# Kernel optimization log

Hardware: AMD Instinct MI355X
Metric: run time of the kernel (lower is better)

The kernel has to match this reference:

```python
import jax, jax.numpy as jnp
import numpy as np
import math

# hyperparams matching init_kwargs
GAMMA_S = 0.8
GAMMA_U = 0.8
RHO_I = 0.1
RHO_T = 0.1
EPS = 1e-10
TAU_MIN = 0.005
TAU_MAX = 1.0
TAU_INIT = 0.07
GRAD_CLIP = 5.0
ETA_INIT = 0.01
ETA_MIN = 0.0001
N_STATE = 2900000
BSZ = 4096
DIM = 1024


def setup_inputs() -> dict:
    key = jax.random.key(0)
    k1, k2 = jax.random.split(key)
    imf = jax.random.normal(k1, (BSZ, DIM), jnp.float32)
    imf = imf / jnp.linalg.norm(imf, axis=1, keepdims=True)
    txf = jax.random.normal(k2, (BSZ, DIM), jnp.float32)
    txf = txf / jnp.linalg.norm(txf, axis=1, keepdims=True)
    return {
        "image_features": imf,
        "text_features": txf,
        "s_I": jnp.zeros((N_STATE,), jnp.float32),
        "s_T": jnp.zeros((N_STATE,), jnp.float32),
        "tau_I": jnp.full((N_STATE,), TAU_INIT, jnp.float32),
        "tau_T": jnp.full((N_STATE,), TAU_INIT, jnp.float32),
        "u_I": jnp.zeros((N_STATE,), jnp.float32),
        "u_T": jnp.zeros((N_STATE,), jnp.float32),
        "b_I": jnp.zeros((N_STATE,), jnp.float32),
        "b_T": jnp.zeros((N_STATE,), jnp.float32),
        "image_ids": jnp.arange(BSZ, dtype=jnp.int32),
        "text_ids": jnp.arange(BSZ, dtype=jnp.int32),
        "epoch": 5,
        "max_epoch": 30,
    }


def reference(image_features, text_features, s_I, s_T, tau_I, tau_T,
              u_I, u_T, b_I, b_T, image_ids, text_ids, epoch, max_epoch):
    B = image_features.shape[0]
    sim = jnp.einsum('id,jd->ij', image_features, text_features)  # [B,B]
    diag_sim = jnp.diagonal(sim)                                  # [B]

    tau_image = tau_I[image_ids]  # [B]
    tau_text = tau_T[text_ids]    # [B]

    image_diffs = sim - diag_sim[:, None]
    text_diffs = sim - diag_sim[None, :]
    # .detach() in torch -> stop_gradient
    idt = jax.lax.stop_gradient(image_diffs / tau_image[:, None])
    tdt = jax.lax.stop_gradient(text_diffs / tau_text[None, :])

    # max-trick state b_I / b_T: running row/col max per sample id
    old_b_I = b_I[image_ids]
    new_b_I = jnp.maximum(jnp.max(idt, axis=1), old_b_I)  # [B]
    old_b_T = b_T[text_ids]
    new_b_T = jnp.maximum(jnp.max(tdt, axis=0), old_b_T)  # [B]

    exp_image_diffs = jnp.exp(idt - new_b_I[:, None])
    exp_text_diffs = jnp.exp(tdt - new_b_T[None, :])
    g_I = jnp.sum(exp_image_diffs, axis=1, keepdims=True) / (B - 1)  # [B,1]
    g_T = jnp.sum(exp_text_diffs, axis=0, keepdims=True) / (B - 1)   # [1,B]

    # moving-average s state (compute_last=False, last_g_* = None path)
    s_I_new = (1.0 - GAMMA_S) * s_I[image_ids] * jnp.exp(old_b_I - new_b_I) + GAMMA_S * g_I[:, 0]
    s_T_new = (1.0 - GAMMA_S) * s_T[text_ids] * jnp.exp(old_b_T - new_b_T) + GAMMA_S * g_T[0, :]
    s_I_b = s_I_new[:, None]  # same shape as g_I
    s_T_b = s_T_new[None, :]  # same shape as g_T

    weights_image = exp_image_diffs / (s_I_b + EPS)
    weights_text = exp_text_diffs / (s_T_b + EPS)

    image_loss = jnp.sum(weights_image * image_diffs, axis=1, keepdims=True) / (B - 1)
    text_loss = jnp.sum(weights_text * text_diffs, axis=0, keepdims=True) / (B - 1)
    total_loss = image_loss.mean() + text_loss.mean()

    grad_tau_image = (jnp.log(s_I_b) + new_b_I[:, None] + RHO_I
                      - jnp.sum(weights_image * idt, axis=1, keepdims=True) / (B - 1))
    grad_tau_text = (jnp.log(s_T_b) + new_b_T[None, :] + RHO_T
                     - jnp.sum(weights_text * tdt, axis=0, keepdims=True) / (B - 1))

    u_I_new = (1.0 - GAMMA_U) * u_I[image_ids] + GAMMA_U * jnp.clip(grad_tau_image[:, 0], -GRAD_CLIP, GRAD_CLIP)
    u_T_new = (1.0 - GAMMA_U) * u_T[text_ids] + GAMMA_U * jnp.clip(grad_tau_text[0, :], -GRAD_CLIP, GRAD_CLIP)

    eta_cur = ETA_MIN + (ETA_INIT - ETA_MIN) * math.cos(math.pi * (epoch / max_epoch) / 2)
    tau_I_new = jnp.clip(tau_image - eta_cur * u_I_new, TAU_MIN, TAU_MAX)
    tau_T_new = jnp.clip(tau_text - eta_cur * u_T_new, TAU_MIN, TAU_MAX)

    # scattered state writes (the module's in-place buffer updates)
    b_I_out = b_I.at[image_ids].set(new_b_I)
    b_T_out = b_T.at[text_ids].set(new_b_T)
    s_I_out = s_I.at[image_ids].set(s_I_new)
    s_T_out = s_T.at[text_ids].set(s_T_new)
    u_I_out = u_I.at[image_ids].set(u_I_new)
    u_T_out = u_T.at[text_ids].set(u_T_new)
    tau_I_out = tau_I.at[image_ids].set(tau_I_new)
    tau_T_out = tau_T.at[text_ids].set(tau_T_new)

    avg_image_tau = tau_image.mean()
    avg_text_tau = tau_text.mean()

    return (g_I, g_T, grad_tau_image, grad_tau_text, total_loss,
            avg_image_tau, avg_text_tau,
            s_I_out, s_T_out, u_I_out, u_T_out,
            b_I_out, b_T_out, tau_I_out, tau_T_out)
```

## Files before the change

### kernel.cpp

```cpp
#include <hip/hip_runtime.h>
#include <math.h>

#define BSZ 4096
#define DIM 1024
#define NST 2900000

constexpr float GAMMA_S   = 0.8f;
constexpr float GAMMA_U   = 0.8f;
constexpr float RHO_I_C   = 0.1f;
constexpr float RHO_T_C   = 0.1f;
constexpr float C_EPS     = 1e-10f;
constexpr float TAU_MIN_C = 0.005f;
constexpr float TAU_MAX_C = 1.0f;
constexpr float GCLIP     = 5.0f;
constexpr float ETA_INIT_C = 0.01f;
constexpr float ETA_MIN_C  = 1e-4f;
constexpr float PI_F       = 3.14159265358979323846f;

typedef __bf16 bf16x8 __attribute__((ext_vector_type(8)));
typedef float  f32x4  __attribute__((ext_vector_type(4)));

__device__ __forceinline__ unsigned short f2bf(float f) {
    unsigned int u = __float_as_uint(f);
    u += 0x7fffu + ((u >> 16) & 1u);
    return (unsigned short)(u >> 16);
}
__device__ __forceinline__ float bf2f(unsigned short s) {
    return __uint_as_float(((unsigned int)s) << 16);
}

__global__ __launch_bounds__(256) void conv_diag(const float* __restrict__ imf,
                                                 const float* __restrict__ txf,
                                                 unsigned short* __restrict__ abf,
                                                 unsigned short* __restrict__ bbf,
                                                 const float* __restrict__ tau_I,
                                                 const float* __restrict__ tau_T,
                                                 const float* __restrict__ b_I,
                                                 const float* __restrict__ b_T,
                                                 const int* __restrict__ iid,
                                                 const int* __restrict__ tid_,
                                                 float* diag, float* tauIg, float* tauTg,
                                                 float* obI, float* obT,
                                                 float* __restrict__ scal) {
    if (blockIdx.x == 0 && threadIdx.x < 3) scal[threadIdx.x] = 0.f;
    const int w  = threadIdx.x >> 6;
    const int ln = threadIdx.x & 63;
    const int i  = blockIdx.x * 4 + w;
    float dot = 0.f;
#pragma unroll
    for (int k = 0; k < 4; ++k) {
        const int off = i * DIM + k * 256 + ln * 4;
        float4 a = *(const float4*)&imf[off];
        float4 b = *(const float4*)&txf[off];
        ushort4 ra, rb;
        ra.x = f2bf(a.x); ra.y = f2bf(a.y); ra.z = f2bf(a.z); ra.w = f2bf(a.w);
        rb.x = f2bf(b.x); rb.y = f2bf(b.y); rb.z = f2bf(b.z); rb.w = f2bf(b.w);
        *(ushort4*)&abf[off] = ra;
        *(ushort4*)&bbf[off] = rb;
        dot += bf2f(ra.x) * bf2f(rb.x) + bf2f(ra.y) * bf2f(rb.y) +
               bf2f(ra.z) * bf2f(rb.z) + bf2f(ra.w) * bf2f(rb.w);
    }
#pragma unroll
    for (int m = 32; m; m >>= 1) dot += __shfl_xor(dot, m);
    if (ln == 0) {
        diag[i] = dot;
        const int id = iid[i];
        tauIg[i] = tau_I[id];
        obI[i]   = b_I[id];
        const int td = tid_[i];
        tauTg[i] = tau_T[td];
        obT[i]   = b_T[td];
    }
}

__device__ __forceinline__ void async16(const void* g, void* l) {
    __builtin_amdgcn_global_load_lds(
        (const __attribute__((address_space(1))) void*)g,
        (__attribute__((address_space(3))) void*)l, 16, 0, 0);
}

__global__ __launch_bounds__(256) void gemm_fused(const unsigned short* __restrict__ A,
                                                  const unsigned short* __restrict__ B,
                                                  const float* __restrict__ diag,
                                                  const float* __restrict__ tauIg,
                                                  const float* __restrict__ tauTg,
                                                  float* __restrict__ rpM,
                                                  float* __restrict__ rpE,
                                                  float* __restrict__ rpV,
                                                  float* __restrict__ cpM,
                                                  float* __restrict__ cpE,
                                                  float* __restrict__ cpV,
                                                  const float* __restrict__ s_I,
                                                  const float* __restrict__ s_T,
                                                  const float* __restrict__ u_I,
                                                  const float* __restrict__ u_T,
                                                  const float* __restrict__ b_I,
                                                  const float* __restrict__ b_T,
                                                  const float* __restrict__ tau_I,
                                                  const float* __restrict__ tau_T,
                                                  float* __restrict__ outbase) {
    __shared__ unsigned short As[128 * 32];
    __shared__ unsigned short Bs[128 * 32];

    const int tid = threadIdx.x;

    if (blockIdx.x >= 1024) {
        const size_t idx = (size_t)(blockIdx.x - 1024) * 256 + tid;
        const size_t stride = (size_t)256 * 256;
        const size_t NV = (NST - 1) / 4;
        const float* srcs[8] = {s_I, s_T, u_I, u_T, b_I, b_T, tau_I, tau_T};
#pragma unroll
        for (int a = 0; a < 8; ++a) {
            const float* s = srcs[a];
            float* d = outbase + (size_t)a * NST;
            for (size_t cidx = idx; cidx < NV; cidx += stride) {
                const size_t e = 1 + 4 * cidx;
                float4 v = make_float4(s[e], s[e + 1], s[e + 2], s[e + 3]);
                *(float4*)&d[e] = v;
            }
            if (idx == 0) d[0] = s[0];
            if (idx < 3)  d[NST - 3 + idx] = s[NST - 3 + idx];
        }
        return;
    }

    const int gid = (blockIdx.x & 7) * 128 + (blockIdx.x >> 3);
    const int bjIdx = gid & 31, biIdx = gid >> 5;
    const int bi = biIdx * 128;
    const int bj = bjIdx * 128;
    const int lane = tid & 63;
    const int wave = tid >> 6;
    const int m_base = (wave >> 1) * 64;
    const int n_base = (wave & 1) * 64;

    const int c0 = tid, c1 = tid + 256;
    const int r0 = c0 >> 2, kg0 = ((c0 & 3) ^ ((r0 >> 1) & 3)) * 8;
    const int r1 = c1 >> 2, kg1 = ((c1 & 3) ^ ((r1 >> 1) & 3)) * 8;

    f32x4 acc[4][4];
#pragma unroll
    for (int m = 0; m < 4; ++m)
#pragma unroll
        for (int n = 0; n < 4; ++n)
            acc[m][n] = (f32x4){0.f, 0.f, 0.f, 0.f};

    const int mrow = lane & 15;
    const int q    = lane >> 4;

    for (int k0 = 0; k0 < DIM; k0 += 32) {
        __syncthreads();
        async16(&A[(size_t)(bi + r0) * DIM + k0 + kg0], &As[c0 * 8]);
        async16(&A[(size_t)(bi + r1) * DIM + k0 + kg1], &As[c1 * 8]);
        async16(&B[(size_t)(bj + r0) * DIM + k0 + kg0], &Bs[c0 * 8]);
        async16(&B[(size_t)(bj + r1) * DIM + k0 + kg1], &Bs[c1 * 8]);
        __syncthreads();

        bf16x8 af[4], bfr[4];
#pragma unroll
        for (int t = 0; t < 4; ++t) {
            const int rlA = m_base + t * 16 + mrow;
            const int rlB = n_base + t * 16 + mrow;
            af[t]  = *(const bf16x8*)&As[rlA * 32 + (q ^ ((rlA >> 1) & 3)) * 8];
            bfr[t] = *(const bf16x8*)&Bs[rlB * 32 + (q ^ ((rlB >> 1) & 3)) * 8];
        }
#pragma unroll
        for (int mt = 0; mt < 4; ++mt)
#pragma unroll
            for (int nt = 0; nt < 4; ++nt)
                acc[mt][nt] = __builtin_amdgcn_mfma_f32_16x16x32_bf16(
                    af[mt], bfr[nt], acc[mt][nt], 0, 0, 0);
    }

    __syncthreads();
    float* prm = (float*)Bs;
    if (tid < 128) {
        prm[tid]       = diag[bi + tid];
        prm[128 + tid] = 1.0f / tauIg[bi + tid];
        prm[256 + tid] = diag[bj + tid];
        prm[384 + tid] = 1.0f / tauTg[bj + tid];
    }
    __syncthreads();

    float* red = (float*)As;
    const int rowq = (lane >> 4) * 4;

#pragma unroll
    for (int mt = 0; mt < 4; ++mt)
#pragma unroll
        for (int r = 0; r < 4; ++r) {
            const int row_l = m_base + mt * 16 + rowq + r;
            const float dgr = prm[row_l];
            const float itr = prm[128 + row_l];
            float v0 = (acc[mt][0][r] - dgr) * itr;
            float v1 = (acc[mt][1][r] - dgr) * itr;
            float v2 = (acc[mt][2][r] - dgr) * itr;
            float v3 = (acc[mt][3][r] - dgr) * itr;
            float m = fmaxf(fmaxf(v0, v1), fmaxf(v2, v3));
#pragma unroll
            for (int x = 1; x <= 8; x <<= 1) m = fmaxf(m, __shfl_xor(m, x));
            const float e0 = __expf(v0 - m), e1 = __expf(v1 - m);
            const float e2 = __expf(v2 - m), e3 = __expf(v3 - m);
            float se = e0 + e1 + e2 + e3;
            float sv = e0 * v0 + e1 * v1 + e2 * v2 + e3 * v3;
#pragma unroll
            for (int x = 1; x <= 8; x <<= 1) {
                se += __shfl_xor(se, x);
                sv += __shfl_xor(sv, x);
            }
            if ((lane & 15) == 0) {
                const int idx = wave * 64 + mt * 16 + rowq + r;
                red[idx] = m; red[256 + idx] = se; red[512 + idx] = sv;
            }
        }

#pragma unroll
    for (int nt = 0; nt < 4; ++nt) {
        const int col_l = n_base + nt * 16 + (lane & 15);
        const float dgc = prm[256 + col_l];
        const float itc = prm[384 + col_l];
        float m = -INFINITY;
#pragma unroll
        for (int mt = 0; mt < 4; ++mt)
#pragma unroll
            for (int r = 0; r < 4; ++r)
                m = fmaxf(m, (acc[mt][nt][r] - dgc) * itc);
        m = fmaxf(m, __shfl_xor(m, 16));
        m = fmaxf(m, __shfl_xor(m, 32));
        float se = 0.f, sv = 0.f;
#pragma unroll
        for (int mt = 0; mt < 4; ++mt)
#pragma unroll
            for (int r = 0; r < 4; ++r) {
                const float v = (acc[mt][nt][r] - dgc) * itc;
                const float e = __expf(v - m);
                se += e; sv += e * v;
            }
        se += __shfl_xor(se, 16); se += __shfl_xor(se, 32);
        sv += __shfl_xor(sv, 16); sv += __shfl_xor(sv, 32);
        if (lane < 16) {
            const int idx = wave * 64 + nt * 16 + lane;
            red[768 + idx] = m; red[1024 + idx] = se; red[1280 + idx] = sv;
        }
    }
    __syncthreads();

    if (tid < 128) {
        const int rg = tid, li = rg & 63;
        const int w0 = (rg >> 6) * 2, w1 = w0 + 1;
        const float mA = red[w0 * 64 + li], mB = red[w1 * 64 + li];
        const float M = fmaxf(mA, mB);
        const float fA = __expf(mA - M), fB = __expf(mB - M);
        const size_t o = (size_t)bjIdx * BSZ + bi + rg;
        rpM[o] = M;
        rpE[o] = red[256 + w0 * 64 + li] * fA + red[256 + w1 * 64 + li] * fB;
        rpV[o] = red[512 + w0 * 64 + li] * fA + red[512 + w1 * 64 + li] * fB;
    } else {
        const int cg = tid - 128, li = cg & 63;
        const int w0 = cg >> 6, w1 = w0 + 2;
        const float mA = red[768 + w0 * 64 + li], mB = red[768 + w1 * 64 + li];
        const float M = fmaxf(mA, mB);
        const float fA = __expf(mA - M), fB = __expf(mB - M);
        const size_t o = (size_t)biIdx * BSZ + bj + cg;
        cpM[o] = M;
        cpE[o] = red[1024 + w0 * 64 + li] * fA + red[1024 + w1 * 64 + li] * fB;
        cpV[o] = red[1280 + w0 * 64 + li] * fA + red[1280 + w1 * 64 + li] * fB;
    }
}

__global__ __launch_bounds__(256) void finalize(const float* __restrict__ s_I,
                                                const float* __restrict__ s_T,
                                                const float* __restrict__ u_I,
                                                const float* __restrict__ u_T,
                                                const int* __restrict__ iid,
                                                const int* __restrict__ tid_,
                                                const int* __restrict__ epoch,
                                                const int* __restrict__ maxep,
                                                const float* __restrict__ tauIg,
                                                const float* __restrict__ tauTg,
                                                const float* __restrict__ obI,
                                                const float* __restrict__ obT,
                                                const float* __restrict__ rpM,
                                                const float* __restrict__ rpE,
                                                const float* __restrict__ rpV,
                                                const float* __restrict__ cpM,
                                                const float* __restrict__ cpE,
                                                const float* __restrict__ cpV,
                                                float* __restrict__ out) {
    const int side = blockIdx.x & 1;
    const int i0   = (blockIdx.x >> 1) * 64;
    const int w    = threadIdx.x >> 6;
    const int il   = threadIdx.x & 63;
    const int i    = i0 + il;

    const float* pM  = side ? cpM  : rpM;
    const float* pE  = side ? cpE  : rpE;
    const float* pV  = side ? cpV  : rpV;
    const float* tg  = side ? tauTg : tauIg;
    const float* obA = side ? obT  : obI;
    const float* sA  = side ? s_T  : s_I;
    const float* uA  = side ? u_T  : u_I;
    const int*   ids = side ? tid_ : iid;
    const float  rho = side ? RHO_T_C : RHO_I_C;

    float M[8], E[8], V[8];
#pragma unroll
    for (int k = 0; k < 8; ++k) {
        const size_t o = (size_t)(w * 8 + k) * BSZ + i;
        M[k] = pM[o]; E[k] = pE[o]; V[k] = pV[o];
    }
    float pm = M[0];
#pragma unroll
    for (int k = 1; k < 8; ++k) pm = fmaxf(pm, M[k]);

    __shared__ float lred[12][64];
    lred[w][il] = pm;
    __syncthreads();

    const float ob = obA[i];
    const float nb = fmaxf(fmaxf(fmaxf(lred[0][il], lred[1][il]),
                                 fmaxf(lred[2][il], lred[3][il])), ob);
    float se = 0.f, sv = 0.f;
#pragma unroll
    for (int k = 0; k < 8; ++k) {
        const float f = __expf(M[k] - nb);
        se += E[k] * f;
        sv += V[k] * f;
    }
    lred[4 + w][il] = se;
    lred[8 + w][il] = sv;
    __syncthreads();

    if (w == 0) {
        const float eta = ETA_MIN_C + (ETA_INIT_C - ETA_MIN_C) *
                          cosf(0.5f * PI_F * ((float)epoch[0] / (float)maxep[0]));
        const float invBm1 = 1.0f / (float)(BSZ - 1);
        const float invB   = 1.0f / (float)BSZ;

        const int   id  = ids[i];
        const float tau = tg[i];
        const float seT = (lred[4][il] + lred[5][il]) + (lred[6][il] + lred[7][il]);
        const float svT = (lred[8][il] + lred[9][il]) + (lred[10][il] + lred[11][il]);

        const float g     = seT * invBm1;
        const float s_new = (1.f - GAMMA_S) * sA[id] * __expf(ob - nb) + GAMMA_S * g;
        const float W     = svT * invBm1 / (s_new + C_EPS);
        const float grad  = logf(s_new) + nb + rho - W;
        const float gc    = fminf(fmaxf(grad, -GCLIP), GCLIP);
        const float u_new = (1.f - GAMMA_U) * uA[id] + GAMMA_U * gc;
        const float tau_new = fminf(fmaxf(tau - eta * u_new, TAU_MIN_C), TAU_MAX_C);

        float* o_g   = out + side * BSZ;
        float* o_gt  = out + (2 + side) * BSZ;
        float* stb   = out + 4 * BSZ + 3;
        float* o_s   = stb + (size_t)side * NST;
        float* o_u   = stb + (size_t)(2 + side) * NST;
        float* o_b   = stb + (size_t)(4 + side) * NST;
        float* o_t   = stb + (size_t)(6 + side) * NST;

        o_g[i]  = g;
        o_gt[i] = grad;
        o_s[id] = s_new;
        o_u[id] = u_new;
        o_b[id] = nb;
        o_t[id] = tau_new;

        float v0 = tau * W * invB;
        float v1 = tau * invB;
#pragma unroll
        for (int o2 = 32; o2; o2 >>= 1) {
            v0 += __shfl_down(v0, o2);
            v1 += __shfl_down(v1, o2);
        }
        if (il == 0) {
            atomicAdd(&out[4 * BSZ + 0], v0);
            atomicAdd(&out[4 * BSZ + 1 + side], v1);
        }
    }
}

extern "C" void kernel_launch(void* const* d_in, const int* in_sizes, int n_in,
                              void* d_out, int out_size, void* d_ws, size_t ws_size,
                              hipStream_t stream) {
    const float* imf   = (const float*)d_in[0];
    const float* txf   = (const float*)d_in[1];
    const float* s_I   = (const float*)d_in[2];
    const float* s_T   = (const float*)d_in[3];
    const float* tau_I = (const float*)d_in[4];
    const float* tau_T = (const float*)d_in[5];
    const float* u_I   = (const float*)d_in[6];
    const float* u_T   = (const float*)d_in[7];
    const float* b_I   = (const float*)d_in[8];
    const float* b_T   = (const float*)d_in[9];
    const int* iid     = (const int*)d_in[10];
    const int* tid_    = (const int*)d_in[11];
    const int* epoch   = (const int*)d_in[12];
    const int* maxep   = (const int*)d_in[13];

    float* out = (float*)d_out;
    float* ws  = (float*)d_ws;

    float* diag  = ws + 0 * BSZ;
    float* tauIg = ws + 1 * BSZ;
    float* tauTg = ws + 2 * BSZ;
    float* obI   = ws + 3 * BSZ;
    float* obT   = ws + 4 * BSZ;
    float* rpM   = ws + 5 * BSZ;
    float* rpE   = rpM + (size_t)32 * BSZ;
    float* rpV   = rpE + (size_t)32 * BSZ;
    float* cpM   = rpV + (size_t)32 * BSZ;
    float* cpE   = cpM + (size_t)32 * BSZ;
    float* cpV   = cpE + (size_t)32 * BSZ;
    unsigned short* abf = (unsigned short*)(cpV + (size_t)32 * BSZ);
    unsigned short* bbf = abf + (size_t)BSZ * DIM;

    conv_diag<<<BSZ / 4, 256, 0, stream>>>(imf, txf, abf, bbf, tau_I, tau_T, b_I, b_T,
                                           iid, tid_, diag, tauIg, tauTg, obI, obT,
                                           out + 4 * BSZ);
    gemm_fused<<<1280, 256, 0, stream>>>(abf, bbf, diag, tauIg, tauTg,
                                         rpM, rpE, rpV, cpM, cpE, cpV,
                                         s_I, s_T, u_I, u_T, b_I, b_T, tau_I, tau_T,
                                         out + 4 * BSZ + 3);
    finalize<<<128, 256, 0, stream>>>(s_I, s_T, u_I, u_T, iid, tid_, epoch, maxep,
                                      tauIg, tauTg, obI, obT,
                                      rpM, rpE, rpV, cpM, cpE, cpV, out);
}
```

Before: 300.8 us.

## Double-buffer GEMM LDS tiles and interleave state-copy blocks with GEMM blocks

The GEMM k-loop now uses two LDS buffers so the async load of the next K slice is issued before the current slice's MFMAs, leaving one barrier per iteration instead of two. The 8-array state copy work moves from 256 trailing blocks to 1024 blocks interleaved with the GEMM blocks in groups of 8, so bandwidth-bound copying runs alongside compute-bound tiles. The copy uses nontemporal loads and stores to keep the large stream out of cache. Doubling LDS may reduce occupancy, and the tile-to-block mapping changes, which affects L2 locality.

```diff
diff --git a/kernel.cpp b/kernel.cpp
--- a/kernel.cpp
+++ b/kernel.cpp
@@ -19,6 +19,7 @@
 
 typedef __bf16 bf16x8 __attribute__((ext_vector_type(8)));
 typedef float  f32x4  __attribute__((ext_vector_type(4)));
+typedef float  f4nt   __attribute__((ext_vector_type(4)));
 
 __device__ __forceinline__ unsigned short f2bf(float f) {
     unsigned int u = __float_as_uint(f);
@@ -99,14 +100,15 @@
                                                   const float* __restrict__ tau_I,
                                                   const float* __restrict__ tau_T,
                                                   float* __restrict__ outbase) {
-    __shared__ unsigned short As[128 * 32];
-    __shared__ unsigned short Bs[128 * 32];
+    __shared__ unsigned short As[2][128 * 32];
+    __shared__ unsigned short Bs[2][128 * 32];
 
     const int tid = threadIdx.x;
-
-    if (blockIdx.x >= 1024) {
-        const size_t idx = (size_t)(blockIdx.x - 1024) * 256 + tid;
-        const size_t stride = (size_t)256 * 256;
+    const int gid = ((blockIdx.x >> 4) << 3) | (blockIdx.x & 7);
+
+    if ((blockIdx.x >> 3) & 1) {
+        const size_t idx = (size_t)gid * 256 + tid;
+        const size_t stride = (size_t)1024 * 256;
         const size_t NV = (NST - 1) / 4;
         const float* srcs[8] = {s_I, s_T, u_I, u_T, b_I, b_T, tau_I, tau_T};
 #pragma unroll
@@ -115,8 +117,12 @@
             float* d = outbase + (size_t)a * NST;
             for (size_t cidx = idx; cidx < NV; cidx += stride) {
                 const size_t e = 1 + 4 * cidx;
-                float4 v = make_float4(s[e], s[e + 1], s[e + 2], s[e + 3]);
-                *(float4*)&d[e] = v;
+                f4nt v;
+                v.x = __builtin_nontemporal_load(&s[e]);
+                v.y = __builtin_nontemporal_load(&s[e + 1]);
+                v.z = __builtin_nontemporal_load(&s[e + 2]);
+                v.w = __builtin_nontemporal_load(&s[e + 3]);
+                __builtin_nontemporal_store(v, (f4nt*)&d[e]);
             }
             if (idx == 0) d[0] = s[0];
             if (idx < 3)  d[NST - 3 + idx] = s[NST - 3 + idx];
@@ -124,7 +130,6 @@
         return;
     }
 
-    const int gid = (blockIdx.x & 7) * 128 + (blockIdx.x >> 3);
     const int bjIdx = gid & 31, biIdx = gid >> 5;
     const int bi = biIdx * 128;
     const int bj = bjIdx * 128;
@@ -147,21 +152,28 @@
     const int mrow = lane & 15;
     const int q    = lane >> 4;
 
-    for (int k0 = 0; k0 < DIM; k0 += 32) {
-        __syncthreads();
-        async16(&A[(size_t)(bi + r0) * DIM + k0 + kg0], &As[c0 * 8]);
-        async16(&A[(size_t)(bi + r1) * DIM + k0 + kg1], &As[c1 * 8]);
-        async16(&B[(size_t)(bj + r0) * DIM + k0 + kg0], &Bs[c0 * 8]);
-        async16(&B[(size_t)(bj + r1) * DIM + k0 + kg1], &Bs[c1 * 8]);
-        __syncthreads();
+#define STG(bufsel, kk0)                                                        \
+    {                                                                           \
+        async16(&A[(size_t)(bi + r0) * DIM + (kk0) + kg0], &As[bufsel][c0 * 8]);\
+        async16(&A[(size_t)(bi + r1) * DIM + (kk0) + kg1], &As[bufsel][c1 * 8]);\
+        async16(&B[(size_t)(bj + r0) * DIM + (kk0) + kg0], &Bs[bufsel][c0 * 8]);\
+        async16(&B[(size_t)(bj + r1) * DIM + (kk0) + kg1], &Bs[bufsel][c1 * 8]);\
+    }
+
+    STG(0, 0);
+    __syncthreads();
+
+    for (int t = 0; t < 32; ++t) {
+        const int cur = t & 1;
+        if (t < 31) STG(cur ^ 1, (t + 1) * 32);
 
         bf16x8 af[4], bfr[4];
 #pragma unroll
-        for (int t = 0; t < 4; ++t) {
-            const int rlA = m_base + t * 16 + mrow;
-            const int rlB = n_base + t * 16 + mrow;
-            af[t]  = *(const bf16x8*)&As[rlA * 32 + (q ^ ((rlA >> 1) & 3)) * 8];
-            bfr[t] = *(const bf16x8*)&Bs[rlB * 32 + (q ^ ((rlB >> 1) & 3)) * 8];
+        for (int tt = 0; tt < 4; ++tt) {
+            const int rlA = m_base + tt * 16 + mrow;
+            const int rlB = n_base + tt * 16 + mrow;
+            af[tt]  = *(const bf16x8*)&As[cur][rlA * 32 + (q ^ ((rlA >> 1) & 3)) * 8];
+            bfr[tt] = *(const bf16x8*)&Bs[cur][rlB * 32 + (q ^ ((rlB >> 1) & 3)) * 8];
         }
 #pragma unroll
         for (int mt = 0; mt < 4; ++mt)
@@ -169,9 +181,11 @@
             for (int nt = 0; nt < 4; ++nt)
                 acc[mt][nt] = __builtin_amdgcn_mfma_f32_16x16x32_bf16(
                     af[mt], bfr[nt], acc[mt][nt], 0, 0, 0);
-    }
-
-    __syncthreads();
+
+        __syncthreads();
+    }
+#undef STG
+
     float* prm = (float*)Bs;
     if (tid < 128) {
         prm[tid]       = diag[bi + tid];
@@ -349,9 +363,9 @@
         const float u_new = (1.f - GAMMA_U) * uA[id] + GAMMA_U * gc;
         const float tau_new = fminf(fmaxf(tau - eta * u_new, TAU_MIN_C), TAU_MAX_C);
 
+        float* stb   = out + 4 * BSZ + 3;
         float* o_g   = out + side * BSZ;
         float* o_gt  = out + (2 + side) * BSZ;
-        float* stb   = out + 4 * BSZ + 3;
         float* o_s   = stb + (size_t)side * NST;
         float* o_u   = stb + (size_t)(2 + side) * NST;
         float* o_b   = stb + (size_t)(4 + side) * NST;
@@ -416,7 +430,7 @@
     conv_diag<<<BSZ / 4, 256, 0, stream>>>(imf, txf, abf, bbf, tau_I, tau_T, b_I, b_T,
                                            iid, tid_, diag, tauIg, tauTg, obI, obT,
                                            out + 4 * BSZ);
-    gemm_fused<<<1280, 256, 0, stream>>>(abf, bbf, diag, tauIg, tauTg,
+    gemm_fused<<<2048, 256, 0, stream>>>(abf, bbf, diag, tauIg, tauTg,
                                          rpM, rpE, rpV, cpM, cpE, cpV,
                                          s_I, s_T, u_I, u_T, b_I, b_T, tau_I, tau_T,
                                          out + 4 * BSZ + 3);
```

Result: no change. 306.4 us (+1.9%).
